# Kernel tuning notes

Hardware: AMD Instinct MI355X
Metric: run time of the kernel (lower is better)

Reference implementation:

```python
import jax, jax.numpy as jnp
import numpy as np

LN_EPS = 1e-5

def _ln(x):
    # haiku LayerNorm([-1], create_scale=False, create_offset=False)
    mu = x.mean(axis=-1, keepdims=True)
    var = x.var(axis=-1, keepdims=True)
    return (x - mu) * jax.lax.rsqrt(var + LN_EPS)

def setup_inputs() -> dict:
    key = jax.random.key(0)
    ks = jax.random.split(key, 10)
    N, L, P = 512, 256, 64
    inp = {
        "local": jax.random.normal(ks[0], (N, L), jnp.float32),
        "pair": jax.random.normal(ks[1], (N, N, P), jnp.float32),
        "mask": jax.random.randint(ks[2], (N,), 0, 2, jnp.int32),
        "W_pair_gate": jax.random.normal(ks[3], (P, 2 * P), jnp.float32) / np.sqrt(P),
        "W_pair_value": jax.random.normal(ks[4], (P, 2 * P), jnp.float32) / np.sqrt(P),
        "W_left_gate": jax.random.normal(ks[5], (L, 2 * P), jnp.float32) / np.sqrt(L),
        "W_left_value": jax.random.normal(ks[6], (L, 2 * P), jnp.float32) / np.sqrt(L),
        "W_right_gate": jax.random.normal(ks[7], (L, 2 * P), jnp.float32) / np.sqrt(L),
        "W_right_value": jax.random.normal(ks[8], (L, 2 * P), jnp.float32) / np.sqrt(L),
        "W_out": jax.random.normal(ks[9], (3 * P, P), jnp.float32) / np.sqrt(3 * P),
    }
    return inp

def reference(local, pair, mask, W_pair_gate, W_pair_value, W_left_gate,
              W_left_value, W_right_gate, W_right_value, W_out):
    maskb = mask.astype(bool)
    pair_mask = maskb[:, None] & maskb[None, :]                  # (N, N)
    l = _ln(local)                                               # (N, L)
    p = _ln(pair)                                                # (N, N, P)
    pair_gate = p @ W_pair_gate                                  # (N, N, 2P)
    pair_value = p @ W_pair_value                                # (N, N, 2P)
    # left: broadcast local over axis 0/1, gelu-gate, mask, reduce over j
    left_gate = jax.nn.gelu((l @ W_left_gate)[:, None] + pair_gate)
    left_value = (l @ W_left_value)[None, :] + pair_value
    left = jnp.where(pair_mask[..., None], left_gate * left_value, 0).sum(axis=1)  # (N, 2P)
    right_gate = jax.nn.gelu((l @ W_right_gate)[None, :] + pair_gate)
    right_value = (l @ W_right_value)[:, None] + pair_value
    right = jnp.where(pair_mask[..., None], right_gate * right_value, 0).sum(axis=0)  # (N, 2P)
    paired_pseudo_local = _ln(left[:, None] + right[None, :])    # (N, N, 2P)
    pair_hidden = jnp.concatenate((p, paired_pseudo_local), axis=-1)  # (N, N, 3P)
    return pair_hidden @ W_out                                   # (N, N, P)
```

## Files before the change

### kernel.cpp

```cpp
#include <hip/hip_runtime.h>
#include <math.h>

#define LN_EPS 1e-5f


typedef __bf16 bf16x8 __attribute__((ext_vector_type(8)));
typedef float f32x16 __attribute__((ext_vector_type(16)));

__device__ __forceinline__ float gelu_f(float x) {
    float x3 = x * x * x;
    float t = 0.7978845608028654f * (x + 0.044715f * x3);
    float e = __expf(2.f * t);
    float th = 1.f - 2.f / (e + 1.f);
    return 0.5f * x * (1.f + th);
}

__global__ __launch_bounds__(256) void kA(
    const float* __restrict__ loc,
    const float* __restrict__ Wlg, const float* __restrict__ Wlv,
    const float* __restrict__ Wrg, const float* __restrict__ Wrv,
    float* __restrict__ proj) {
    __shared__ float ln_sh[8][260];
    __shared__ float red_sh[128][9];
    const int t = threadIdx.x;
    const int i0 = blockIdx.x * 8;
    const int mat = blockIdx.y;
    const float* __restrict__ W = (mat == 0) ? Wlg : (mat == 1) ? Wlv
                                 : (mat == 2) ? Wrg : Wrv;
    {
        int row = t >> 5, l32 = t & 31;
        const float4* src = (const float4*)(loc + (i0 + row) * 256);
        float4 v0 = src[l32 * 2];
        float4 v1 = src[l32 * 2 + 1];
        float s = (v0.x + v0.y) + (v0.z + v0.w) + (v1.x + v1.y) + (v1.z + v1.w);
        float ss = v0.x * v0.x + v0.y * v0.y + v0.z * v0.z + v0.w * v0.w +
                   v1.x * v1.x + v1.y * v1.y + v1.z * v1.z + v1.w * v1.w;
#pragma unroll
        for (int off = 1; off < 32; off <<= 1) {
            s += __shfl_xor(s, off);
            ss += __shfl_xor(ss, off);
        }
        float mu = s * (1.f / 256.f);
        float rs = rsqrtf(ss * (1.f / 256.f) - mu * mu + LN_EPS);
        float4 o0, o1;
        o0.x = (v0.x - mu) * rs; o0.y = (v0.y - mu) * rs;
        o0.z = (v0.z - mu) * rs; o0.w = (v0.w - mu) * rs;
        o1.x = (v1.x - mu) * rs; o1.y = (v1.y - mu) * rs;
        o1.z = (v1.z - mu) * rs; o1.w = (v1.w - mu) * rs;
        *(float4*)&ln_sh[row][l32 * 8] = o0;
        *(float4*)&ln_sh[row][l32 * 8 + 4] = o1;
    }
    __syncthreads();

    const int n = t & 127;
    const int kh = t >> 7;
    float acc[8] = {0.f, 0.f, 0.f, 0.f, 0.f, 0.f, 0.f, 0.f};
#pragma unroll 2
    for (int c = 0; c < 32; ++c) {
        const int kc = kh * 128 + c * 4;
        float w0 = W[(kc + 0) * 128 + n];
        float w1 = W[(kc + 1) * 128 + n];
        float w2 = W[(kc + 2) * 128 + n];
        float w3 = W[(kc + 3) * 128 + n];
#pragma unroll
        for (int r = 0; r < 8; ++r) {
            float4 l4 = *(const float4*)&ln_sh[r][kc];
            acc[r] += l4.x * w0 + l4.y * w1 + l4.z * w2 + l4.w * w3;
        }
    }
    if (kh == 1) {
#pragma unroll
        for (int r = 0; r < 8; ++r) red_sh[n][r] = acc[r];
    }
    __syncthreads();
    if (kh == 0) {
#pragma unroll
        for (int r = 0; r < 8; ++r)
            proj[mat * 65536 + (i0 + r) * 128 + n] = acc[r] + red_sh[n][r];
    }
}

#define KB_TI 8
__global__ __launch_bounds__(256, 2) void kB(
    const float* __restrict__ pair, const int* __restrict__ mask,
    const float* __restrict__ Wg, const float* __restrict__ Wv,
    const float* __restrict__ lg, const float* __restrict__ lv,
    const float* __restrict__ rg, const float* __restrict__ rv,
    float* __restrict__ left, float* __restrict__ right) {
    __shared__ __bf16 A_sh[32][72];
    __shared__ float lv_sh[32][132];
    __shared__ float rg_sh[32][132];
    __shared__ float mj_sh[32];

    const int t = threadIdx.x;
    const int lane = t & 63;
    const int w = t >> 6;
    const int j0 = blockIdx.x * 32;
    const int i0 = blockIdx.y * KB_TI;
    const int c = lane & 31;
    const int half = lane >> 5;
    const int mbase = 4 * half;

    bf16x8 bfrag[2][4];
#pragma unroll
    for (int tt = 0; tt < 2; ++tt) {
        int C = (2 * w + tt) * 32 + c;
        int n = C >> 1;
        const float* Wsrc = (C & 1) ? Wv : Wg;
#pragma unroll
        for (int kt = 0; kt < 4; ++kt) {
            bf16x8 v;
#pragma unroll
            for (int e = 0; e < 8; ++e)
                v[e] = (__bf16)Wsrc[(kt * 16 + half * 8 + e) * 128 + n];
            bfrag[tt][kt] = v;
        }
    }

    for (int idx = t; idx < 1024; idx += 256) {
        int row = idx >> 5, n4 = (idx & 31) * 4;
        *(float4*)&lv_sh[row][n4] = *(const float4*)(lv + (j0 + row) * 128 + n4);
        *(float4*)&rg_sh[row][n4] = *(const float4*)(rg + (j0 + row) * 128 + n4);
    }
    if (t < 32) mj_sh[t] = (float)mask[j0 + t];
    __syncthreads();

    float mjv[16];
#pragma unroll
    for (int r = 0; r < 16; ++r)
        mjv[r] = mj_sh[mbase + (r & 3) + 8 * (r >> 2)];

    float racc[2][16];
#pragma unroll
    for (int tt = 0; tt < 2; ++tt)
#pragma unroll
        for (int r = 0; r < 16; ++r) racc[tt][r] = 0.f;

    const int evencol = !(c & 1);

    for (int ii = 0; ii < KB_TI; ++ii) {
        const int i = i0 + ii;
        if (mask[i] == 0) continue;
        __syncthreads();
        {
            int row = t >> 3;
            int kc = (t & 7) * 8;
            const float* src = pair + ((size_t)i * 512 + j0 + row) * 64 + kc;
            float4 v0 = *(const float4*)src;
            float4 v1 = *(const float4*)(src + 4);
            float s = (v0.x + v0.y) + (v0.z + v0.w) + (v1.x + v1.y) + (v1.z + v1.w);
            float ss = v0.x * v0.x + v0.y * v0.y + v0.z * v0.z + v0.w * v0.w +
                       v1.x * v1.x + v1.y * v1.y + v1.z * v1.z + v1.w * v1.w;
            s += __shfl_xor(s, 1); ss += __shfl_xor(ss, 1);
            s += __shfl_xor(s, 2); ss += __shfl_xor(ss, 2);
            s += __shfl_xor(s, 4); ss += __shfl_xor(ss, 4);
            float mu = s * (1.f / 64.f);
            float rs = rsqrtf(ss * (1.f / 64.f) - mu * mu + LN_EPS);
            bf16x8 o;
            o[0] = (__bf16)((v0.x - mu) * rs); o[1] = (__bf16)((v0.y - mu) * rs);
            o[2] = (__bf16)((v0.z - mu) * rs); o[3] = (__bf16)((v0.w - mu) * rs);
            o[4] = (__bf16)((v1.x - mu) * rs); o[5] = (__bf16)((v1.y - mu) * rs);
            o[6] = (__bf16)((v1.z - mu) * rs); o[7] = (__bf16)((v1.w - mu) * rs);
            *(bf16x8*)&A_sh[row][kc] = o;
        }
        __syncthreads();

        f32x16 acc0 = {}; f32x16 acc1 = {};
#pragma unroll
        for (int kt = 0; kt < 4; ++kt) {
            bf16x8 af = *(const bf16x8*)&A_sh[c][kt * 16 + half * 8];
            acc0 = __builtin_amdgcn_mfma_f32_32x32x16_bf16(af, bfrag[0][kt], acc0, 0, 0, 0);
            acc1 = __builtin_amdgcn_mfma_f32_32x32x16_bf16(af, bfrag[1][kt], acc1, 0, 0, 0);
        }

#pragma unroll
        for (int tt = 0; tt < 2; ++tt) {
            int n = (((2 * w + tt) * 32) + c) >> 1;
            float lgi = lg[i * 128 + n];
            float rvi = rv[i * 128 + n];
            float lsum = 0.f;
#pragma unroll
            for (int r = 0; r < 16; ++r) {
                int m = mbase + (r & 3) + 8 * (r >> 2);
                float v = tt ? acc1[r] : acc0[r];
                float pp = __shfl_xor(v, 1);
                float lvm = lv_sh[m][n];
                float rgm = rg_sh[m][n];
                float gb = evencol ? lgi : rgm;
                float vb = evencol ? lvm : rvi;
                float pg = evencol ? v : pp;
                float pv = evencol ? pp : v;
                float res = gelu_f(gb + pg) * (vb + pv);
                lsum += res * mjv[r];
                racc[tt][r] += res;
            }
            float tot = lsum + __shfl_xor(lsum, 32);
            if (evencol && lane < 32) atomicAdd(&left[i * 128 + n], tot);
        }
    }

    if (!evencol) {
#pragma unroll
        for (int tt = 0; tt < 2; ++tt) {
            int n = (((2 * w + tt) * 32) + c) >> 1;
#pragma unroll
            for (int r = 0; r < 16; ++r) {
                int m = mbase + (r & 3) + 8 * (r >> 2);
                atomicAdd(&right[(j0 + m) * 128 + n], racc[tt][r] * mjv[r]);
            }
        }
    }
}

__global__ void kD1(const float* __restrict__ left, const float* __restrict__ right,
                    const float* __restrict__ W_out,
                    float* __restrict__ Aw, float* __restrict__ Bw,
                    float* __restrict__ sums, float* __restrict__ cs) {
    const int t = threadIdx.x;
    const int r = blockIdx.x;
    const int which = blockIdx.y;
    const float* src = which ? right : left;
    __shared__ float row_sh[128];
    __shared__ float red[4];
    float v = src[r * 128 + t];
    row_sh[t] = v;
    float s = v, ss = v * v;
#pragma unroll
    for (int off = 1; off < 64; off <<= 1) {
        s += __shfl_xor(s, off);
        ss += __shfl_xor(ss, off);
    }
    int wid = t >> 6, lane = t & 63;
    if (lane == 0) { red[wid * 2] = s; red[wid * 2 + 1] = ss; }
    __syncthreads();
    if (t == 0) {
        sums[which * 1024 + r] = red[0] + red[2];
        sums[which * 1024 + 512 + r] = red[1] + red[3];
    }
    if (t < 64) {
        float a = 0.f;
        const float* W2 = W_out + 64 * 64;
#pragma unroll 8
        for (int m = 0; m < 128; ++m) a += row_sh[m] * W2[m * 64 + t];
        (which ? Bw : Aw)[r * 64 + t] = a;
    }
    if (r == 0 && which == 0 && t < 64) {
        float c0 = 0.f, c1 = 0.f;
        for (int k = 0; k < 64; ++k) c0 += W_out[k * 64 + t];
        for (int m = 0; m < 128; ++m) c1 += W_out[(64 + m) * 64 + t];
        cs[t] = c0;
        cs[64 + t] = c1;
    }
}

__global__ void kD2(const float* __restrict__ left, const float* __restrict__ right,
                    float* __restrict__ C) {
    __shared__ float l_sh[32][68];
    __shared__ float r_sh[32][68];
    const int t = threadIdx.x;
    const int tx = t & 15, ty = t >> 4;
    const int i0 = blockIdx.x * 32, j0 = blockIdx.y * 32;
    float acc00 = 0.f, acc01 = 0.f, acc10 = 0.f, acc11 = 0.f;
    for (int kc = 0; kc < 128; kc += 64) {
        __syncthreads();
#pragma unroll
        for (int u = 0; u < 2; ++u) {
            int fi = t + u * 256;
            int row = fi >> 4, kq = (fi & 15) * 4;
            float4 lv4 = *(const float4*)(left + (i0 + row) * 128 + kc + kq);
            float4 rv4 = *(const float4*)(right + (j0 + row) * 128 + kc + kq);
            *(float4*)&l_sh[row][kq] = lv4;
            *(float4*)&r_sh[row][kq] = rv4;
        }
        __syncthreads();
#pragma unroll 8
        for (int k = 0; k < 64; ++k) {
            float l0 = l_sh[ty * 2 + 0][k], l1 = l_sh[ty * 2 + 1][k];
            float r0 = r_sh[tx * 2 + 0][k], r1 = r_sh[tx * 2 + 1][k];
            acc00 += l0 * r0; acc01 += l0 * r1;
            acc10 += l1 * r0; acc11 += l1 * r1;
        }
    }
    C[(size_t)(i0 + ty * 2 + 0) * 512 + j0 + tx * 2 + 0] = acc00;
    C[(size_t)(i0 + ty * 2 + 0) * 512 + j0 + tx * 2 + 1] = acc01;
    C[(size_t)(i0 + ty * 2 + 1) * 512 + j0 + tx * 2 + 0] = acc10;
    C[(size_t)(i0 + ty * 2 + 1) * 512 + j0 + tx * 2 + 1] = acc11;
}

__global__ __launch_bounds__(256, 2) void kC(
    const float* __restrict__ pair, const float* __restrict__ Wout,
    const float* __restrict__ Aw, const float* __restrict__ Bw,
    const float* __restrict__ Cw, const float* __restrict__ sums,
    const float* __restrict__ cs, float* __restrict__ out) {
    __shared__ __bf16 A_sh[64][72];
    __shared__ float B_sh[64][68];
    __shared__ float Cv_sh[64];
    __shared__ float sR_sh[64];
    __shared__ float ssR_sh[64];

    const int t = threadIdx.x;
    const int lane = t & 63;
    const int w = t >> 6;
    const int i = blockIdx.x;
    const int j0 = blockIdx.y * 64;
    const int c = lane & 31;
    const int half = lane >> 5;
    const int mt = w & 1;
    const int nt = w >> 1;
    const int n = nt * 32 + c;

    bf16x8 bfrag[4];
#pragma unroll
    for (int kt = 0; kt < 4; ++kt) {
        bf16x8 v;
#pragma unroll
        for (int e = 0; e < 8; ++e)
            v[e] = (__bf16)Wout[(kt * 16 + half * 8 + e) * 64 + n];
        bfrag[kt] = v;
    }

    for (int idx = t; idx < 1024; idx += 256) {
        int row = idx >> 4, n4 = (idx & 15) * 4;
        *(float4*)&B_sh[row][n4] = *(const float4*)(Bw + (j0 + row) * 64 + n4);
    }
    if (t < 64) {
        Cv_sh[t] = Cw[(size_t)i * 512 + j0 + t];
        sR_sh[t] = sums[1024 + j0 + t];
        ssR_sh[t] = sums[1536 + j0 + t];
    }
    {
        int row = t >> 2;
        int kc = (t & 3) * 16;
        const float* src = pair + ((size_t)i * 512 + j0 + row) * 64 + kc;
        float4 v0 = *(const float4*)src;
        float4 v1 = *(const float4*)(src + 4);
        float4 v2 = *(const float4*)(src + 8);
        float4 v3 = *(const float4*)(src + 12);
        float s = (v0.x + v0.y + v0.z + v0.w) + (v1.x + v1.y + v1.z + v1.w) +
                  (v2.x + v2.y + v2.z + v2.w) + (v3.x + v3.y + v3.z + v3.w);
        float ss = v0.x * v0.x + v0.y * v0.y + v0.z * v0.z + v0.w * v0.w +
                   v1.x * v1.x + v1.y * v1.y + v1.z * v1.z + v1.w * v1.w +
                   v2.x * v2.x + v2.y * v2.y + v2.z * v2.z + v2.w * v2.w +
                   v3.x * v3.x + v3.y * v3.y + v3.z * v3.z + v3.w * v3.w;
        s += __shfl_xor(s, 1); ss += __shfl_xor(ss, 1);
        s += __shfl_xor(s, 2); ss += __shfl_xor(ss, 2);
        float mu = s * (1.f / 64.f);
        float rs = rsqrtf(ss * (1.f / 64.f) - mu * mu + LN_EPS);
        bf16x8 o0, o1;
        o0[0] = (__bf16)((v0.x - mu) * rs); o0[1] = (__bf16)((v0.y - mu) * rs);
        o0[2] = (__bf16)((v0.z - mu) * rs); o0[3] = (__bf16)((v0.w - mu) * rs);
        o0[4] = (__bf16)((v1.x - mu) * rs); o0[5] = (__bf16)((v1.y - mu) * rs);
        o0[6] = (__bf16)((v1.z - mu) * rs); o0[7] = (__bf16)((v1.w - mu) * rs);
        o1[0] = (__bf16)((v2.x - mu) * rs); o1[1] = (__bf16)((v2.y - mu) * rs);
        o1[2] = (__bf16)((v2.z - mu) * rs); o1[3] = (__bf16)((v2.w - mu) * rs);
        o1[4] = (__bf16)((v3.x - mu) * rs); o1[5] = (__bf16)((v3.y - mu) * rs);
        o1[6] = (__bf16)((v3.z - mu) * rs); o1[7] = (__bf16)((v3.w - mu) * rs);
        *(bf16x8*)&A_sh[row][kc] = o0;
        *(bf16x8*)&A_sh[row][kc + 8] = o1;
    }
    __syncthreads();

    f32x16 acc = {};
#pragma unroll
    for (int kt = 0; kt < 4; ++kt) {
        bf16x8 af = *(const bf16x8*)&A_sh[mt * 32 + c][kt * 16 + half * 8];
        acc = __builtin_amdgcn_mfma_f32_32x32x16_bf16(af, bfrag[kt], acc, 0, 0, 0);
    }

    const float sumLi = sums[i], ssLi = sums[512 + i];
    const float A_in = Aw[i * 64 + n];
    const float cs1n = cs[64 + n];

#pragma unroll
    for (int r = 0; r < 16; ++r) {
        int m = mt * 32 + 4 * half + (r & 3) + 8 * (r >> 2);
        float Bv = B_sh[m][n];
        float Cv = Cv_sh[m];
        float mu_s = (sumLi + sR_sh[m]) * (1.f / 128.f);
        float var_s = (ssLi + 2.f * Cv + ssR_sh[m]) * (1.f / 128.f) - mu_s * mu_s;
        float rs_s = rsqrtf(var_s + LN_EPS);
        out[((size_t)i * 512 + j0 + m) * 64 + n] = acc[r] + rs_s * (A_in + Bv - mu_s * cs1n);
    }
}

extern "C" void kernel_launch(void* const* d_in, const int* in_sizes, int n_in,
                              void* d_out, int out_size, void* d_ws, size_t ws_size,
                              hipStream_t stream) {
    const float* loc  = (const float*)d_in[0];
    const float* pair = (const float*)d_in[1];
    const int*   mask = (const int*)d_in[2];
    const float* Wpg  = (const float*)d_in[3];
    const float* Wpv  = (const float*)d_in[4];
    const float* Wlg  = (const float*)d_in[5];
    const float* Wlv  = (const float*)d_in[6];
    const float* Wrg  = (const float*)d_in[7];
    const float* Wrv  = (const float*)d_in[8];
    const float* Wout = (const float*)d_in[9];
    float* out = (float*)d_out;
    float* ws = (float*)d_ws;

    float* proj  = ws;
    float* left  = ws + 262144;
    float* right = ws + 327680;
    float* Aw    = ws + 393216;
    float* Bw    = ws + 425984;
    float* Cw    = ws + 458752;
    float* sums  = ws + 720896;
    float* cs    = ws + 722944;

    hipMemsetAsync(left, 0, 2 * 65536 * sizeof(float), stream);

    kA<<<dim3(64, 4), 256, 0, stream>>>(loc, Wlg, Wlv, Wrg, Wrv, proj);
    kB<<<dim3(16, 512 / KB_TI), 256, 0, stream>>>(pair, mask, Wpg, Wpv,
                                                  proj, proj + 65536, proj + 131072,
                                                  proj + 196608, left, right);
    kD1<<<dim3(512, 2), 128, 0, stream>>>(left, right, Wout, Aw, Bw, sums, cs);
    kD2<<<dim3(16, 16), 256, 0, stream>>>(left, right, Cw);
    kC<<<dim3(512, 8), 256, 0, stream>>>(pair, Wout, Aw, Bw, Cw, sums, cs, out);
}
```

Baseline: 228.7 us.

## Compact masked indices, double-buffer kB, fast GELU, and restructure kC for two rows

A new kernel compacts the mask into a list of active indices, and kB then iterates only over active i/j pairs, so masked pairs are skipped in both dimensions instead of only in i. kB is also restructured with separate gate and value MFMAs, double-buffered shared A tiles with prefetch of the next pair row, and no shuffle-based column pairing. GELU uses an exp2/rcp form of the tanh approximation. kC processes two i rows per block with precomputed per-pair LN scale terms, reading Bw directly from global memory; this adds register pressure and gives up the occupancy launch bound.

```diff
diff --git a/kernel.cpp b/kernel.cpp
--- a/kernel.cpp
+++ b/kernel.cpp
@@ -8,11 +8,25 @@
 typedef float f32x16 __attribute__((ext_vector_type(16)));
 
 __device__ __forceinline__ float gelu_f(float x) {
-    float x3 = x * x * x;
-    float t = 0.7978845608028654f * (x + 0.044715f * x3);
-    float e = __expf(2.f * t);
-    float th = 1.f - 2.f / (e + 1.f);
-    return 0.5f * x * (1.f + th);
+    float x2 = x * x;
+    float e = __builtin_amdgcn_exp2f(x * fmaf(0.10294423f, x2, 2.3022079f));
+    float r = __builtin_amdgcn_rcpf(e + 1.0f);
+    return fmaf(-x, r, x);
+}
+
+__global__ void kM(const int* __restrict__ mask, int* __restrict__ act) {
+    const int t = threadIdx.x;
+    const int lane = t & 63, w = t >> 6;
+    __shared__ int wcnt_sh[8];
+    int m = (mask[t] != 0);
+    unsigned long long b = __ballot(m);
+    if (lane == 0) wcnt_sh[w] = __popcll(b);
+    __syncthreads();
+    int base = 0;
+    for (int u = 0; u < w; ++u) base += wcnt_sh[u];
+    int pos = base + __popcll(b & ((1ull << lane) - 1ull));
+    if (m) act[1 + pos] = t;
+    if (t == 511) act[0] = base + __popcll(b);
 }
 
 __global__ __launch_bounds__(256) void kA(
@@ -81,134 +95,134 @@
 }
 
 #define KB_TI 8
-__global__ __launch_bounds__(256, 2) void kB(
-    const float* __restrict__ pair, const int* __restrict__ mask,
+__global__ __launch_bounds__(256) void kB(
+    const float* __restrict__ pair, const int* __restrict__ act,
     const float* __restrict__ Wg, const float* __restrict__ Wv,
     const float* __restrict__ lg, const float* __restrict__ lv,
     const float* __restrict__ rg, const float* __restrict__ rv,
     float* __restrict__ left, float* __restrict__ right) {
-    __shared__ __bf16 A_sh[32][72];
+    __shared__ __bf16 A_sh[2][32][72];
     __shared__ float lv_sh[32][132];
     __shared__ float rg_sh[32][132];
-    __shared__ float mj_sh[32];
+    __shared__ int ji_sh[32];
+    __shared__ int ii_sh[KB_TI];
+
+    const int cnt = act[0];
+    const int j0 = blockIdx.x * 32;
+    const int ibase = blockIdx.y * KB_TI;
+    if (j0 >= cnt || ibase >= cnt) return;
+    const int nact = min(KB_TI, cnt - ibase);
 
     const int t = threadIdx.x;
     const int lane = t & 63;
     const int w = t >> 6;
-    const int j0 = blockIdx.x * 32;
-    const int i0 = blockIdx.y * KB_TI;
     const int c = lane & 31;
     const int half = lane >> 5;
-    const int mbase = 4 * half;
-
-    bf16x8 bfrag[2][4];
-#pragma unroll
-    for (int tt = 0; tt < 2; ++tt) {
-        int C = (2 * w + tt) * 32 + c;
-        int n = C >> 1;
-        const float* Wsrc = (C & 1) ? Wv : Wg;
+    const int n = w * 32 + c;
+
+    if (t < 32) ji_sh[t] = act[1 + min(j0 + t, cnt - 1)];
+    if (t >= 64 && t < 64 + KB_TI) ii_sh[t - 64] = act[1 + min(ibase + (t - 64), cnt - 1)];
+    __syncthreads();
+
+    bf16x8 bg[4], bv[4];
+#pragma unroll
+    for (int kt = 0; kt < 4; ++kt) {
+        bf16x8 vg, vv;
+#pragma unroll
+        for (int e = 0; e < 8; ++e) {
+            int kr = kt * 16 + half * 8 + e;
+            vg[e] = (__bf16)Wg[kr * 128 + n];
+            vv[e] = (__bf16)Wv[kr * 128 + n];
+        }
+        bg[kt] = vg; bv[kt] = vv;
+    }
+
+    for (int idx = t; idx < 32 * 128; idx += 256) {
+        int jj = idx >> 7, nn = idx & 127;
+        int j = ji_sh[jj];
+        lv_sh[jj][nn] = lv[j * 128 + nn];
+        rg_sh[jj][nn] = rg[j * 128 + nn];
+    }
+
+    const int srow = t >> 3;
+    const int kseg = (t & 7) * 8;
+    float4 p0, p1;
+    float plg, prv;
+
+    {
+        int iF = act[1 + ibase];
+        const float* src = pair + ((size_t)iF * 512 + ji_sh[srow]) * 64 + kseg;
+        p0 = *(const float4*)src;
+        p1 = *(const float4*)(src + 4);
+        plg = lg[iF * 128 + n];
+        prv = rv[iF * 128 + n];
+    }
+
+    auto lnwrite = [&](int buf) {
+        float s = (p0.x + p0.y) + (p0.z + p0.w) + (p1.x + p1.y) + (p1.z + p1.w);
+        float ss = p0.x * p0.x + p0.y * p0.y + p0.z * p0.z + p0.w * p0.w +
+                   p1.x * p1.x + p1.y * p1.y + p1.z * p1.z + p1.w * p1.w;
+        s += __shfl_xor(s, 1); ss += __shfl_xor(ss, 1);
+        s += __shfl_xor(s, 2); ss += __shfl_xor(ss, 2);
+        s += __shfl_xor(s, 4); ss += __shfl_xor(ss, 4);
+        float mu = s * (1.f / 64.f);
+        float rs = rsqrtf(ss * (1.f / 64.f) - mu * mu + LN_EPS);
+        bf16x8 o;
+        o[0] = (__bf16)((p0.x - mu) * rs); o[1] = (__bf16)((p0.y - mu) * rs);
+        o[2] = (__bf16)((p0.z - mu) * rs); o[3] = (__bf16)((p0.w - mu) * rs);
+        o[4] = (__bf16)((p1.x - mu) * rs); o[5] = (__bf16)((p1.y - mu) * rs);
+        o[6] = (__bf16)((p1.z - mu) * rs); o[7] = (__bf16)((p1.w - mu) * rs);
+        *(bf16x8*)&A_sh[buf][srow][kseg] = o;
+    };
+    lnwrite(0);
+    __syncthreads();
+
+    float racc[16];
+#pragma unroll
+    for (int r = 0; r < 16; ++r) racc[r] = 0.f;
+
+    for (int ii = 0; ii < nact; ++ii) {
+        const int i = ii_sh[ii];
+        const float lgi = plg;
+        const float rvi = prv;
+        if (ii + 1 < nact) {
+            int iF = ii_sh[ii + 1];
+            const float* src = pair + ((size_t)iF * 512 + ji_sh[srow]) * 64 + kseg;
+            p0 = *(const float4*)src;
+            p1 = *(const float4*)(src + 4);
+            plg = lg[iF * 128 + n];
+            prv = rv[iF * 128 + n];
+        }
+
+        f32x16 ag = {}; f32x16 av = {};
 #pragma unroll
         for (int kt = 0; kt < 4; ++kt) {
-            bf16x8 v;
-#pragma unroll
-            for (int e = 0; e < 8; ++e)
-                v[e] = (__bf16)Wsrc[(kt * 16 + half * 8 + e) * 128 + n];
-            bfrag[tt][kt] = v;
-        }
-    }
-
-    for (int idx = t; idx < 1024; idx += 256) {
-        int row = idx >> 5, n4 = (idx & 31) * 4;
-        *(float4*)&lv_sh[row][n4] = *(const float4*)(lv + (j0 + row) * 128 + n4);
-        *(float4*)&rg_sh[row][n4] = *(const float4*)(rg + (j0 + row) * 128 + n4);
-    }
-    if (t < 32) mj_sh[t] = (float)mask[j0 + t];
-    __syncthreads();
-
-    float mjv[16];
-#pragma unroll
-    for (int r = 0; r < 16; ++r)
-        mjv[r] = mj_sh[mbase + (r & 3) + 8 * (r >> 2)];
-
-    float racc[2][16];
-#pragma unroll
-    for (int tt = 0; tt < 2; ++tt)
-#pragma unroll
-        for (int r = 0; r < 16; ++r) racc[tt][r] = 0.f;
-
-    const int evencol = !(c & 1);
-
-    for (int ii = 0; ii < KB_TI; ++ii) {
-        const int i = i0 + ii;
-        if (mask[i] == 0) continue;
+            bf16x8 af = *(const bf16x8*)&A_sh[ii & 1][c][kt * 16 + half * 8];
+            ag = __builtin_amdgcn_mfma_f32_32x32x16_bf16(af, bg[kt], ag, 0, 0, 0);
+            av = __builtin_amdgcn_mfma_f32_32x32x16_bf16(af, bv[kt], av, 0, 0, 0);
+        }
+
+        float lsum = 0.f;
+#pragma unroll
+        for (int r = 0; r < 16; ++r) {
+            int m = 4 * half + (r & 3) + 8 * (r >> 2);
+            float pg = ag[r], pv = av[r];
+            float lres = gelu_f(lgi + pg) * (lv_sh[m][n] + pv);
+            float rres = gelu_f(rg_sh[m][n] + pg) * (rvi + pv);
+            if (j0 + m < cnt) lsum += lres;
+            racc[r] += rres;
+        }
+        float tot = lsum + __shfl_xor(lsum, 32);
+        if (lane < 32) atomicAdd(&left[i * 128 + n], tot);
+
+        if (ii + 1 < nact) lnwrite((ii + 1) & 1);
         __syncthreads();
-        {
-            int row = t >> 3;
-            int kc = (t & 7) * 8;
-            const float* src = pair + ((size_t)i * 512 + j0 + row) * 64 + kc;
-            float4 v0 = *(const float4*)src;
-            float4 v1 = *(const float4*)(src + 4);
-            float s = (v0.x + v0.y) + (v0.z + v0.w) + (v1.x + v1.y) + (v1.z + v1.w);
-            float ss = v0.x * v0.x + v0.y * v0.y + v0.z * v0.z + v0.w * v0.w +
-                       v1.x * v1.x + v1.y * v1.y + v1.z * v1.z + v1.w * v1.w;
-            s += __shfl_xor(s, 1); ss += __shfl_xor(ss, 1);
-            s += __shfl_xor(s, 2); ss += __shfl_xor(ss, 2);
-            s += __shfl_xor(s, 4); ss += __shfl_xor(ss, 4);
-            float mu = s * (1.f / 64.f);
-            float rs = rsqrtf(ss * (1.f / 64.f) - mu * mu + LN_EPS);
-            bf16x8 o;
-            o[0] = (__bf16)((v0.x - mu) * rs); o[1] = (__bf16)((v0.y - mu) * rs);
-            o[2] = (__bf16)((v0.z - mu) * rs); o[3] = (__bf16)((v0.w - mu) * rs);
-            o[4] = (__bf16)((v1.x - mu) * rs); o[5] = (__bf16)((v1.y - mu) * rs);
-            o[6] = (__bf16)((v1.z - mu) * rs); o[7] = (__bf16)((v1.w - mu) * rs);
-            *(bf16x8*)&A_sh[row][kc] = o;
-        }
-        __syncthreads();
-
-        f32x16 acc0 = {}; f32x16 acc1 = {};
-#pragma unroll
-        for (int kt = 0; kt < 4; ++kt) {
-            bf16x8 af = *(const bf16x8*)&A_sh[c][kt * 16 + half * 8];
-            acc0 = __builtin_amdgcn_mfma_f32_32x32x16_bf16(af, bfrag[0][kt], acc0, 0, 0, 0);
-            acc1 = __builtin_amdgcn_mfma_f32_32x32x16_bf16(af, bfrag[1][kt], acc1, 0, 0, 0);
-        }
-
-#pragma unroll
-        for (int tt = 0; tt < 2; ++tt) {
-            int n = (((2 * w + tt) * 32) + c) >> 1;
-            float lgi = lg[i * 128 + n];
-            float rvi = rv[i * 128 + n];
-            float lsum = 0.f;
-#pragma unroll
-            for (int r = 0; r < 16; ++r) {
-                int m = mbase + (r & 3) + 8 * (r >> 2);
-                float v = tt ? acc1[r] : acc0[r];
-                float pp = __shfl_xor(v, 1);
-                float lvm = lv_sh[m][n];
-                float rgm = rg_sh[m][n];
-                float gb = evencol ? lgi : rgm;
-                float vb = evencol ? lvm : rvi;
-                float pg = evencol ? v : pp;
-                float pv = evencol ? pp : v;
-                float res = gelu_f(gb + pg) * (vb + pv);
-                lsum += res * mjv[r];
-                racc[tt][r] += res;
-            }
-            float tot = lsum + __shfl_xor(lsum, 32);
-            if (evencol && lane < 32) atomicAdd(&left[i * 128 + n], tot);
-        }
-    }
-
-    if (!evencol) {
-#pragma unroll
-        for (int tt = 0; tt < 2; ++tt) {
-            int n = (((2 * w + tt) * 32) + c) >> 1;
-#pragma unroll
-            for (int r = 0; r < 16; ++r) {
-                int m = mbase + (r & 3) + 8 * (r >> 2);
-                atomicAdd(&right[(j0 + m) * 128 + n], racc[tt][r] * mjv[r]);
-            }
-        }
+    }
+
+#pragma unroll
+    for (int r = 0; r < 16; ++r) {
+        int m = 4 * half + (r & 3) + 8 * (r >> 2);
+        if (j0 + m < cnt) atomicAdd(&right[ji_sh[m] * 128 + n], racc[r]);
     }
 }
 
@@ -287,99 +301,109 @@
     C[(size_t)(i0 + ty * 2 + 1) * 512 + j0 + tx * 2 + 1] = acc11;
 }
 
-__global__ __launch_bounds__(256, 2) void kC(
+__global__ __launch_bounds__(256) void kC(
     const float* __restrict__ pair, const float* __restrict__ Wout,
     const float* __restrict__ Aw, const float* __restrict__ Bw,
     const float* __restrict__ Cw, const float* __restrict__ sums,
     const float* __restrict__ cs, float* __restrict__ out) {
-    __shared__ __bf16 A_sh[64][72];
-    __shared__ float B_sh[64][68];
-    __shared__ float Cv_sh[64];
-    __shared__ float sR_sh[64];
-    __shared__ float ssR_sh[64];
+    __shared__ __bf16 A_sh[2][64][72];
+    __shared__ float rs_sh[128], q_sh[128];
 
     const int t = threadIdx.x;
     const int lane = t & 63;
     const int w = t >> 6;
-    const int i = blockIdx.x;
-    const int j0 = blockIdx.y * 64;
     const int c = lane & 31;
     const int half = lane >> 5;
-    const int mt = w & 1;
+    const int i0 = blockIdx.x * 2;
+    const int j0 = blockIdx.y * 64;
+    const int isub = w & 1;
     const int nt = w >> 1;
     const int n = nt * 32 + c;
-
-    bf16x8 bfrag[4];
+    const int i = i0 + isub;
+
+    bf16x8 bo[4];
 #pragma unroll
     for (int kt = 0; kt < 4; ++kt) {
         bf16x8 v;
 #pragma unroll
         for (int e = 0; e < 8; ++e)
             v[e] = (__bf16)Wout[(kt * 16 + half * 8 + e) * 64 + n];
-        bfrag[kt] = v;
-    }
-
-    for (int idx = t; idx < 1024; idx += 256) {
-        int row = idx >> 4, n4 = (idx & 15) * 4;
-        *(float4*)&B_sh[row][n4] = *(const float4*)(Bw + (j0 + row) * 64 + n4);
-    }
-    if (t < 64) {
-        Cv_sh[t] = Cw[(size_t)i * 512 + j0 + t];
-        sR_sh[t] = sums[1024 + j0 + t];
-        ssR_sh[t] = sums[1536 + j0 + t];
+        bo[kt] = v;
+    }
+
+    if (t < 128) {
+        int ip = i0 + (t >> 6);
+        int jp = j0 + (t & 63);
+        float sumL = sums[ip], ssL = sums[512 + ip];
+        float sR = sums[1024 + jp], ssR = sums[1536 + jp];
+        float Cv = Cw[(size_t)ip * 512 + jp];
+        float mu = (sumL + sR) * (1.f / 128.f);
+        float var = (ssL + 2.f * Cv + ssR) * (1.f / 128.f) - mu * mu;
+        float rs = rsqrtf(var + LN_EPS);
+        rs_sh[t] = rs;
+        q_sh[t] = rs * mu;
     }
     {
-        int row = t >> 2;
-        int kc = (t & 3) * 16;
-        const float* src = pair + ((size_t)i * 512 + j0 + row) * 64 + kc;
-        float4 v0 = *(const float4*)src;
-        float4 v1 = *(const float4*)(src + 4);
-        float4 v2 = *(const float4*)(src + 8);
-        float4 v3 = *(const float4*)(src + 12);
-        float s = (v0.x + v0.y + v0.z + v0.w) + (v1.x + v1.y + v1.z + v1.w) +
-                  (v2.x + v2.y + v2.z + v2.w) + (v3.x + v3.y + v3.z + v3.w);
-        float ss = v0.x * v0.x + v0.y * v0.y + v0.z * v0.z + v0.w * v0.w +
-                   v1.x * v1.x + v1.y * v1.y + v1.z * v1.z + v1.w * v1.w +
-                   v2.x * v2.x + v2.y * v2.y + v2.z * v2.z + v2.w * v2.w +
-                   v3.x * v3.x + v3.y * v3.y + v3.z * v3.z + v3.w * v3.w;
+        int row = t >> 1;
+        int kc = (t & 1) * 32;
+        const float* src = pair + ((size_t)(i0 + (row >> 6)) * 512 + j0 + (row & 63)) * 64 + kc;
+        float4 v[8];
+#pragma unroll
+        for (int u = 0; u < 8; ++u) v[u] = ((const float4*)src)[u];
+        float s = 0.f, ss = 0.f;
+#pragma unroll
+        for (int u = 0; u < 8; ++u) {
+            s += (v[u].x + v[u].y) + (v[u].z + v[u].w);
+            ss += v[u].x * v[u].x + v[u].y * v[u].y + v[u].z * v[u].z + v[u].w * v[u].w;
+        }
         s += __shfl_xor(s, 1); ss += __shfl_xor(ss, 1);
-        s += __shfl_xor(s, 2); ss += __shfl_xor(ss, 2);
         float mu = s * (1.f / 64.f);
         float rs = rsqrtf(ss * (1.f / 64.f) - mu * mu + LN_EPS);
-        bf16x8 o0, o1;
-        o0[0] = (__bf16)((v0.x - mu) * rs); o0[1] = (__bf16)((v0.y - mu) * rs);
-        o0[2] = (__bf16)((v0.z - mu) * rs); o0[3] = (__bf16)((v0.w - mu) * rs);
-        o0[4] = (__bf16)((v1.x - mu) * rs); o0[5] = (__bf16)((v1.y - mu) * rs);
-        o0[6] = (__bf16)((v1.z - mu) * rs); o0[7] = (__bf16)((v1.w - mu) * rs);
-        o1[0] = (__bf16)((v2.x - mu) * rs); o1[1] = (__bf16)((v2.y - mu) * rs);
-        o1[2] = (__bf16)((v2.z - mu) * rs); o1[3] = (__bf16)((v2.w - mu) * rs);
-        o1[4] = (__bf16)((v3.x - mu) * rs); o1[5] = (__bf16)((v3.y - mu) * rs);
-        o1[6] = (__bf16)((v3.z - mu) * rs); o1[7] = (__bf16)((v3.w - mu) * rs);
-        *(bf16x8*)&A_sh[row][kc] = o0;
-        *(bf16x8*)&A_sh[row][kc + 8] = o1;
-    }
-    __syncthreads();
-
-    f32x16 acc = {};
+#pragma unroll
+        for (int u = 0; u < 2; ++u) {
+            bf16x8 o;
+            o[0] = (__bf16)((v[u*2].x - mu) * rs);   o[1] = (__bf16)((v[u*2].y - mu) * rs);
+            o[2] = (__bf16)((v[u*2].z - mu) * rs);   o[3] = (__bf16)((v[u*2].w - mu) * rs);
+            o[4] = (__bf16)((v[u*2+1].x - mu) * rs); o[5] = (__bf16)((v[u*2+1].y - mu) * rs);
+            o[6] = (__bf16)((v[u*2+1].z - mu) * rs); o[7] = (__bf16)((v[u*2+1].w - mu) * rs);
+            *(bf16x8*)&A_sh[row >> 6][row & 63][kc + u * 8] = o;
+        }
+#pragma unroll
+        for (int u = 2; u < 4; ++u) {
+            bf16x8 o;
+            o[0] = (__bf16)((v[u*2].x - mu) * rs);   o[1] = (__bf16)((v[u*2].y - mu) * rs);
+            o[2] = (__bf16)((v[u*2].z - mu) * rs);   o[3] = (__bf16)((v[u*2].w - mu) * rs);
+            o[4] = (__bf16)((v[u*2+1].x - mu) * rs); o[5] = (__bf16)((v[u*2+1].y - mu) * rs);
+            o[6] = (__bf16)((v[u*2+1].z - mu) * rs); o[7] = (__bf16)((v[u*2+1].w - mu) * rs);
+            *(bf16x8*)&A_sh[row >> 6][row & 63][kc + u * 8] = o;
+        }
+    }
+    __syncthreads();
+
+    f32x16 acc0 = {}; f32x16 acc1 = {};
 #pragma unroll
     for (int kt = 0; kt < 4; ++kt) {
-        bf16x8 af = *(const bf16x8*)&A_sh[mt * 32 + c][kt * 16 + half * 8];
-        acc = __builtin_amdgcn_mfma_f32_32x32x16_bf16(af, bfrag[kt], acc, 0, 0, 0);
-    }
-
-    const float sumLi = sums[i], ssLi = sums[512 + i];
+        bf16x8 a0 = *(const bf16x8*)&A_sh[isub][c][kt * 16 + half * 8];
+        bf16x8 a1 = *(const bf16x8*)&A_sh[isub][32 + c][kt * 16 + half * 8];
+        acc0 = __builtin_amdgcn_mfma_f32_32x32x16_bf16(a0, bo[kt], acc0, 0, 0, 0);
+        acc1 = __builtin_amdgcn_mfma_f32_32x32x16_bf16(a1, bo[kt], acc1, 0, 0, 0);
+    }
+
     const float A_in = Aw[i * 64 + n];
     const float cs1n = cs[64 + n];
 
 #pragma unroll
-    for (int r = 0; r < 16; ++r) {
-        int m = mt * 32 + 4 * half + (r & 3) + 8 * (r >> 2);
-        float Bv = B_sh[m][n];
-        float Cv = Cv_sh[m];
-        float mu_s = (sumLi + sR_sh[m]) * (1.f / 128.f);
-        float var_s = (ssLi + 2.f * Cv + ssR_sh[m]) * (1.f / 128.f) - mu_s * mu_s;
-        float rs_s = rsqrtf(var_s + LN_EPS);
-        out[((size_t)i * 512 + j0 + m) * 64 + n] = acc[r] + rs_s * (A_in + Bv - mu_s * cs1n);
+    for (int mt = 0; mt < 2; ++mt) {
+#pragma unroll
+        for (int r = 0; r < 16; ++r) {
+            int m = mt * 32 + 4 * half + (r & 3) + 8 * (r >> 2);
+            float a = mt ? acc1[r] : acc0[r];
+            float Bv = Bw[(j0 + m) * 64 + n];
+            float rs = rs_sh[isub * 64 + m];
+            float q = q_sh[isub * 64 + m];
+            out[((size_t)i * 512 + j0 + m) * 64 + n] =
+                fmaf(rs, A_in + Bv, fmaf(-q, cs1n, a));
+        }
     }
 }
 
@@ -407,14 +431,16 @@
     float* Cw    = ws + 458752;
     float* sums  = ws + 720896;
     float* cs    = ws + 722944;
+    int*   act   = (int*)(ws + 723072);
 
     hipMemsetAsync(left, 0, 2 * 65536 * sizeof(float), stream);
 
+    kM<<<1, 512, 0, stream>>>(mask, act);
     kA<<<dim3(64, 4), 256, 0, stream>>>(loc, Wlg, Wlv, Wrg, Wrv, proj);
-    kB<<<dim3(16, 512 / KB_TI), 256, 0, stream>>>(pair, mask, Wpg, Wpv,
-                                                  proj, proj + 65536, proj + 131072,
-                                                  proj + 196608, left, right);
+    kB<<<dim3(16, 64), 256, 0, stream>>>(pair, act, Wpg, Wpv,
+                                         proj, proj + 65536, proj + 131072,
+                                         proj + 196608, left, right);
     kD1<<<dim3(512, 2), 128, 0, stream>>>(left, right, Wout, Aw, Bw, sums, cs);
     kD2<<<dim3(16, 16), 256, 0, stream>>>(left, right, Cw);
-    kC<<<dim3(512, 8), 256, 0, stream>>>(pair, Wout, Aw, Bw, Cw, sums, cs, out);
-}
+    kC<<<dim3(256, 8), 256, 0, stream>>>(pair, Wout, Aw, Bw, Cw, sums, cs, out);
+}
```

Result: faster. 198.7 us (-13.1%).
